# Optimization experiments

Hardware: AMD Instinct MI355X
Metric: run time of the kernel (lower is better)

## Reference

```python
import jax, jax.numpy as jnp
import numpy as np

B, T, DF, S = 64, 16, 512, 196      # batch, ticks, backbone channels, tokens
D_IN, H = 512, 8                     # attention embed dim, heads
DH = D_IN // H
DM, MEM, HN = 1024, 25, 32           # d_model neurons, memory length, NLM hidden
NSA, NSO, DOUT = 512, 512, 512       # sync sizes (random-pairing), output dim


def _ln(x, g, b, eps=1e-5):
    m = x.mean(-1, keepdims=True)
    v = ((x - m) ** 2).mean(-1, keepdims=True)
    return (x - m) / jnp.sqrt(v + eps) * g + b


def setup_inputs() -> dict:
    key = jax.random.key(0)
    ks = jax.random.split(key, 24)
    rn = lambda k, sh, sc: jax.random.normal(k, sh, jnp.float32) * sc
    p = {}
    p['x'] = rn(ks[0], (B, T, DF, S), 1.0)
    # q_proj (LazyLinear: n_sync_action -> d_input)
    p['Wqp'] = rn(ks[1], (NSA, D_IN), (1.0 / NSA) ** 0.5); p['bqp'] = jnp.zeros((D_IN,))
    # kv_proj: LazyLinear(DF->D_IN) + LayerNorm
    p['Wkv'] = rn(ks[2], (DF, D_IN), (1.0 / DF) ** 0.5); p['bkv'] = jnp.zeros((D_IN,))
    p['g_kv'] = jnp.ones((D_IN,)); p['b_kv'] = jnp.zeros((D_IN,))
    # MultiheadAttention projections
    sc = (1.0 / D_IN) ** 0.5
    p['Wq'] = rn(ks[3], (D_IN, D_IN), sc); p['bq'] = jnp.zeros((D_IN,))
    p['Wk'] = rn(ks[4], (D_IN, D_IN), sc); p['bk'] = jnp.zeros((D_IN,))
    p['Wv'] = rn(ks[5], (D_IN, D_IN), sc); p['bv'] = jnp.zeros((D_IN,))
    p['Wo'] = rn(ks[6], (D_IN, D_IN), sc); p['bo'] = jnp.zeros((D_IN,))
    # synapses: Linear(D_IN+DM -> 2*DM) + GLU + LayerNorm(DM)
    p['Wsyn'] = rn(ks[7], (D_IN + DM, 2 * DM), (1.0 / (D_IN + DM)) ** 0.5)
    p['bsyn'] = jnp.zeros((2 * DM,))
    p['g_syn'] = jnp.ones((DM,)); p['b_syn'] = jnp.zeros((DM,))
    # NLM: per-neuron 2-layer MLP over memory window
    p['W1'] = rn(ks[8], (DM, MEM, HN), (1.0 / MEM) ** 0.5); p['b1'] = jnp.zeros((DM, HN))
    p['W2'] = rn(ks[9], (DM, HN), (1.0 / HN) ** 0.5); p['b2'] = jnp.zeros((DM,))
    # learned initial states
    p['init_act'] = rn(ks[10], (DM,), (1.0 / DM) ** 0.5)
    p['init_hist'] = rn(ks[11], (DM, MEM), (1.0 / (DM + MEM)) ** 0.5)
    # decay params (init zero in torch)
    p['decay_a'] = jnp.zeros((NSA,)); p['decay_o'] = jnp.zeros((NSO,))
    # output projection (LazyLinear: n_sync_out -> d_output)
    p['Wout'] = rn(ks[12], (NSO, DOUT), (1.0 / NSO) ** 0.5); p['bout'] = jnp.zeros((DOUT,))
    # random-pairing neuron indices (buffers, constants)
    p['li_a'] = jax.random.randint(ks[13], (NSA,), 0, DM, jnp.int32)
    p['ri_a'] = jax.random.randint(ks[14], (NSA,), 0, DM, jnp.int32)
    p['li_o'] = jax.random.randint(ks[15], (NSO,), 0, DM, jnp.int32)
    p['ri_o'] = jax.random.randint(ks[16], (NSO,), 0, DM, jnp.int32)
    return p


def reference(x, Wqp, bqp, Wkv, bkv, g_kv, b_kv, Wq, bq, Wk, bk, Wv, bv, Wo, bo,
              Wsyn, bsyn, g_syn, b_syn, W1, b1, W2, b2, init_act, init_hist,
              decay_a, decay_o, Wout, bout, li_a, ri_a, li_o, ri_o):
    r_a = jnp.exp(-jnp.clip(decay_a, 0.0, 15.0))   # [NSA]
    r_o = jnp.exp(-jnp.clip(decay_o, 0.0, 15.0))   # [NSO]
    act0 = jnp.broadcast_to(init_act, (B, DM))
    hist0 = jnp.broadcast_to(init_hist, (B, DM, MEM))
    # initial 'out' sync state (decay_alpha=pairwise, decay_beta=ones)
    ao0 = act0[:, li_o] * act0[:, ri_o]
    bo0 = jnp.ones_like(ao0)
    # 'action' state starts None -> zeros so first update gives alpha=pairwise, beta=1
    aa0 = jnp.zeros((B, NSA), x.dtype); ba0 = jnp.zeros((B, NSA), x.dtype)

    def mha(q, kv):
        # q [B,1,D_IN], kv [B,S,D_IN]
        qh = (q @ Wq + bq).reshape(B, 1, H, DH)
        kh = (kv @ Wk + bk).reshape(B, S, H, DH)
        vh = (kv @ Wv + bv).reshape(B, S, H, DH)
        sc = jnp.einsum('bqhd,bkhd->bhqk', qh, kh) / jnp.sqrt(jnp.float32(DH))
        a = jax.nn.softmax(sc, axis=-1)
        o = jnp.einsum('bhqk,bkhd->bqhd', a, vh).reshape(B, 1, D_IN)
        return o @ Wo + bo

    def tick(carry, xt):
        act, hist, aa, ba, ao, bo_ = carry
        # compute_kv: identity backbone, flatten(2).transpose(1,2) -> [B,S,DF]
        kv = _ln(jnp.swapaxes(xt, 1, 2) @ Wkv + bkv, g_kv, b_kv)
        # action sync
        aa = r_a * aa + act[:, li_a] * act[:, ri_a]
        ba = r_a * ba + 1.0
        sync_a = aa / jnp.sqrt(ba)
        q = (sync_a @ Wqp + bqp)[:, None, :]
        attn = mha(q, kv)[:, 0]                         # [B,D_IN]
        pre = jnp.concatenate([attn, act], axis=-1)     # [B,D_IN+DM]
        g = pre @ Wsyn + bsyn
        a_, b_ = jnp.split(g, 2, axis=-1)
        pre_act = _ln(a_ * jax.nn.sigmoid(b_), g_syn, b_syn)  # [B,DM]
        hist = jnp.concatenate([hist[:, :, 1:], pre_act[:, :, None]], axis=2)
        # NLM: per-neuron MLP over memory window
        h = jax.nn.relu(jnp.einsum('bnm,nmh->bnh', hist, W1) + b1)
        act = jnp.einsum('bnh,nh->bn', h, W2) + b2
        # out sync
        ao = r_o * ao + act[:, li_o] * act[:, ri_o]
        bo_ = r_o * bo_ + 1.0
        sync_o = ao / jnp.sqrt(bo_)
        pred = sync_o @ Wout + bout                      # [B,DOUT]
        logp = jax.nn.log_softmax(pred, axis=-1)
        ne = -(jnp.exp(logp) * logp).sum(-1) / jnp.log(jnp.float32(DOUT))
        cert = jnp.stack([ne, 1.0 - ne], axis=-1)        # [B,2]
        return (act, hist, aa, ba, ao, bo_), (pred, cert)

    xt = jnp.moveaxis(x, 1, 0)  # [T,B,DF,S]
    _, (preds, certs) = jax.lax.scan(tick, (act0, hist0, aa0, ba0, ao0, bo0), xt)
    predictions = jnp.moveaxis(preds, 0, -1)   # [B,DOUT,T]
    certainties = jnp.moveaxis(certs, 0, -1)   # [B,2,T]
    return predictions, certainties
```

## Files before the change

### kernel.cpp

```cpp
#include <hip/hip_runtime.h>
#include <stdint.h>
#include <stddef.h>

#define B_    64
#define T_    16
#define DF_   512
#define S_    196
#define DIN_  512
#define H_    8
#define DH_   64
#define DM_   1024
#define MEM_  25
#define HN_   32
#define MR_   (B_*S_)

typedef short bf16x8 __attribute__((ext_vector_type(8)));
typedef short short4v __attribute__((ext_vector_type(4)));
typedef float f32x4  __attribute__((ext_vector_type(4)));

__device__ __forceinline__ float b2f(short h){
  unsigned u = ((unsigned)(unsigned short)h) << 16;
  float f; __builtin_memcpy(&f, &u, 4); return f;
}
__device__ __forceinline__ short f2b(float f){
  unsigned u; __builtin_memcpy(&u, &f, 4);
  u = (u + 0x7fffu + ((u >> 16) & 1u)) >> 16;
  return (short)(unsigned short)u;
}
__device__ __forceinline__ float clip015(float d){
  return d < 0.f ? 0.f : (d > 15.f ? 15.f : d);
}

template<int OUTF32, int LNEPI>
__global__ __launch_bounds__(256,2) void gemm_k(
    const short* __restrict__ A, const short* __restrict__ WT,
    void* __restrict__ Cout,
    const float* __restrict__ biasA, const float* __restrict__ biasB, int nsplit,
    const float* __restrict__ mu, const float* __restrict__ iv,
    const float* __restrict__ gw, const float* __restrict__ bw,
    int M, int N, int K, int lda, int ldc)
{
  __shared__ short lA[128*64];
  __shared__ short lB[128*64];
  const int tid = threadIdx.x;
  const int w = tid >> 6, l = tid & 63;
  const int m0 = blockIdx.x * 128, n0 = blockIdx.y * 128;
  const int wm = (w >> 1) * 64, wn = (w & 1) * 64;
  f32x4 acc[4][4];
  #pragma unroll
  for (int i=0;i<4;i++)
    #pragma unroll
    for (int j=0;j<4;j++) acc[i][j] = (f32x4){0.f,0.f,0.f,0.f};

  for (int k0 = 0; k0 < K; k0 += 64) {
    #pragma unroll
    for (int rnd = 0; rnd < 4; ++rnd) {
      int cb = (rnd*4 + w) * 64;
      int slot = cb + l;
      int row = slot >> 3, kb = slot & 7;
      int kc = k0 + ((kb ^ (row & 7)) << 3);
      int gm = m0 + row; if (gm > M-1) gm = M-1;
      __builtin_amdgcn_global_load_lds(
          (const __attribute__((address_space(1))) void*)(A + (size_t)gm * lda + kc),
          (__attribute__((address_space(3))) void*)&lA[cb*8], 16, 0, 0);
      __builtin_amdgcn_global_load_lds(
          (const __attribute__((address_space(1))) void*)(WT + (size_t)(n0 + row) * K + kc),
          (__attribute__((address_space(3))) void*)&lB[cb*8], 16, 0, 0);
    }
    asm volatile("s_waitcnt vmcnt(0)" ::: "memory");
    __syncthreads();
    #pragma unroll
    for (int ks = 0; ks < 2; ++ks) {
      bf16x8 af[4], bfr[4];
      #pragma unroll
      for (int i = 0; i < 4; ++i) {
        int ra = wm + i*16 + (l & 15);
        int c  = ks*4 + (l >> 4);
        af[i]  = *(const bf16x8*)&lA[ra*64 + ((c ^ (ra & 7)) << 3)];
        int rb = wn + i*16 + (l & 15);
        bfr[i] = *(const bf16x8*)&lB[rb*64 + ((c ^ (rb & 7)) << 3)];
      }
      #pragma unroll
      for (int i = 0; i < 4; ++i)
        #pragma unroll
        for (int j = 0; j < 4; ++j)
          acc[i][j] = __builtin_amdgcn_mfma_f32_16x16x32_bf16(af[i], bfr[j], acc[i][j], 0, 0, 0);
    }
    __syncthreads();
  }
  #pragma unroll
  for (int i = 0; i < 4; ++i) {
    #pragma unroll
    for (int j = 0; j < 4; ++j) {
      int gn = n0 + wn + j*16 + (l & 15);
      float ivn = 0.f, mun = 0.f, bb = 0.f;
      if (LNEPI == 2) { ivn = iv[gn]; mun = mu[gn]; }
      else bb = biasA ? ((gn < nsplit) ? biasA[gn] : biasB[gn - nsplit]) : 0.f;
      #pragma unroll
      for (int r = 0; r < 4; ++r) {
        int gm = m0 + wm + i*16 + (l >> 4)*4 + r;
        if (gm < M) {
          float v;
          if (LNEPI == 2) v = ivn*(acc[i][j][r] - mun*gw[gm]) + bw[gm];
          else            v = acc[i][j][r] + bb;
          if (OUTF32) ((float*)Cout)[(size_t)gm * ldc + gn] = v;
          else        ((short*)Cout)[(size_t)gm * ldc + gn] = f2b(v);
        }
      }
    }
  }
}

__global__ __launch_bounds__(256) void xpose_x(const float* __restrict__ x,
                                               short* __restrict__ xT, int t0, int tc)
{
  __shared__ float tile[32][33];
  int df0 = blockIdx.x*32, s0 = blockIdx.y*32;
  int z = blockIdx.z;
  int b = z / tc, ti = z % tc;
  int tx = threadIdx.x & 31, ty = threadIdx.x >> 5;
  const float* src = x + (size_t)(b*T_ + t0 + ti) * DF_ * S_;
  #pragma unroll
  for (int i = 0; i < 4; ++i) {
    int df = df0 + ty + i*8;
    int s  = s0 + tx;
    tile[ty+i*8][tx] = (s < S_) ? src[(size_t)df*S_ + s] : 0.f;
  }
  __syncthreads();
  short* dst = xT + (size_t)(ti*B_ + b) * S_ * DIN_;
  #pragma unroll
  for (int i = 0; i < 4; ++i) {
    int s  = s0 + ty + i*8;
    int df = df0 + tx;
    if (s < S_) dst[(size_t)s*DF_ + df] = f2b(tile[tx][ty+i*8]);
  }
}

__global__ __launch_bounds__(256) void wtrans(const float* __restrict__ in,
    short* __restrict__ out, int R, int C, int ldo, int coff,
    const float* __restrict__ scale)
{
  __shared__ float tile[32][33];
  int c0 = blockIdx.x*32, r0 = blockIdx.y*32;
  int tx = threadIdx.x & 31, ty = threadIdx.x >> 5;
  #pragma unroll
  for (int i = 0; i < 4; ++i) {
    int r = r0+ty+i*8;
    float sc = scale ? scale[r] : 1.f;
    tile[ty+i*8][tx] = in[(size_t)r*C + c0+tx] * sc;
  }
  __syncthreads();
  #pragma unroll
  for (int i = 0; i < 4; ++i)
    out[(size_t)(c0+ty+i*8)*ldo + coff + r0+tx] = f2b(tile[tx][ty+i*8]);
}

__global__ __launch_bounds__(256) void cvtb(const float* __restrict__ in,
                                            short* __restrict__ out, int n)
{
  int i = blockIdx.x*256 + threadIdx.x;
  if (i < n) out[i] = f2b(in[i]);
}

__global__ __launch_bounds__(256) void bias_fold(const float* __restrict__ vec,
    const float* __restrict__ W, const float* __restrict__ base,
    float* __restrict__ out, int N, int ldw)
{
  int n = blockIdx.x*256 + threadIdx.x;
  if (n >= N) return;
  float a = base ? base[n] : 0.f;
  #pragma unroll 8
  for (int k = 0; k < 512; ++k) a += vec[k]*W[(size_t)k*ldw + n];
  out[n] = a;
}

__global__ __launch_bounds__(256) void permrows(const short* __restrict__ in,
                                                short* __restrict__ out)
{
  int r = blockIdx.x;
  int k = r >> 4, i = r & 15;
  int src = (i < 8) ? (k*8 + i) : (1024 + k*8 + (i - 8));
  const bf16x8* s = (const bf16x8*)(in + (size_t)src*1536);
  bf16x8* d = (bf16x8*)(out + (size_t)r*1536);
  int j = threadIdx.x;
  if (j < 192) d[j] = s[j];
}

__global__ __launch_bounds__(256) void ln_stats(const short* __restrict__ in,
    float* __restrict__ mu, float* __restrict__ iv, int nrows)
{
  int w = threadIdx.x >> 6, l = threadIdx.x & 63;
  int r = blockIdx.x*4 + w;
  if (r >= nrows) return;
  bf16x8 v8 = *(const bf16x8*)&in[(size_t)r*512 + l*8];
  float s = 0.f, s2 = 0.f;
  #pragma unroll
  for (int j = 0; j < 8; ++j) { float v = b2f(v8[j]); s += v; s2 += v*v; }
  #pragma unroll
  for (int m = 1; m < 64; m <<= 1) { s += __shfl_xor(s, m, 64); s2 += __shfl_xor(s2, m, 64); }
  if (l == 0) {
    float mean = s * (1.f/512.f);
    float var  = s2 * (1.f/512.f) - mean*mean;
    mu[r] = mean;
    iv[r] = rsqrtf(var + 1e-5f);
  }
}

__device__ __forceinline__ void outk_body(int tt, int b, int tid,
    float* syncL, float* wred,
    const float* actT, float* ao, float* bo_s,
    const int* li_o, const int* ri_o, const float* decay_o,
    const short* WoutB, const float* bout, float* out)
{
  int j = tid;
  float rr = expf(-clip015(decay_o[j]));
  float prod = actT[li_o[j]*64 + b] * actT[ri_o[j]*64 + b];
  float a2 = rr*ao[b*512+j] + prod; ao[b*512+j] = a2;
  float bb2 = rr*bo_s[b*512+j] + 1.f; bo_s[b*512+j] = bb2;
  syncL[j] = a2 * rsqrtf(bb2);
  __syncthreads();
  float a = bout[j];
  #pragma unroll 8
  for (int k = 0; k < 512; ++k) a += syncL[k]*b2f(WoutB[k*512+j]);
  out[((size_t)b*512 + j)*16 + tt] = a;
  int w = tid >> 6, l = tid & 63;
  float m = a;
  #pragma unroll
  for (int k = 32; k >= 1; k >>= 1) m = fmaxf(m, __shfl_xor(m, k, 64));
  if (l == 0) wred[w] = m;
  __syncthreads();
  float M = wred[0];
  #pragma unroll
  for (int k = 1; k < 8; ++k) M = fmaxf(M, wred[k]);
  float e = expf(a - M);
  float z = e, s1 = e*(a - M);
  #pragma unroll
  for (int k = 32; k >= 1; k >>= 1) { z += __shfl_xor(z, k, 64); s1 += __shfl_xor(s1, k, 64); }
  if (l == 0) { wred[8+w] = z; wred[16+w] = s1; }
  __syncthreads();
  if (tid == 0) {
    float Z = 0.f, S1 = 0.f;
    #pragma unroll
    for (int k = 0; k < 8; ++k) { Z += wred[8+k]; S1 += wred[16+k]; }
    float plp = S1 / Z - logf(Z);
    float ne = -plp * (1.f/logf(512.f));
    out[524288 + (size_t)b*32 + tt]      = ne;
    out[524288 + (size_t)b*32 + 16 + tt] = 1.f - ne;
  }
}

__global__ __launch_bounds__(512) void tick_ao(
    const float* __restrict__ actT,
    float* __restrict__ aa, float* __restrict__ ba,
    const int* __restrict__ li_a, const int* __restrict__ ri_a,
    const float* __restrict__ decay_a,
    const short* __restrict__ WqqB, const float* __restrict__ bqh,
    const short* __restrict__ KVT, int ldkv, int ti,
    short* __restrict__ preb,
    float* __restrict__ ao, float* __restrict__ bo_s,
    const int* __restrict__ li_o, const int* __restrict__ ri_o,
    const float* __restrict__ decay_o,
    const short* __restrict__ WoutB, const float* __restrict__ bout,
    float* __restrict__ out, int t)
{
  __shared__ __attribute__((aligned(16))) float smem[3072];
  const int bid = blockIdx.x, tid = threadIdx.x;
  if (bid < 64) {
    int b = bid;
    float* syncL = smem;
    float* qhL   = smem + 512;
    float* pL    = smem + 1024;
    int j = tid;
    float rr = expf(-clip015(decay_a[j]));
    float prod = actT[li_a[j]*64 + b] * actT[ri_a[j]*64 + b];
    float a2 = rr*aa[b*512+j] + prod; aa[b*512+j] = a2;
    float bb2 = rr*ba[b*512+j] + 1.f;  ba[b*512+j] = bb2;
    syncL[j] = a2 * rsqrtf(bb2);
    __syncthreads();
    float qa = bqh[j];
    #pragma unroll 8
    for (int k = 0; k < 512; ++k) qa += syncL[k]*b2f(WqqB[k*512+j]);
    qhL[j] = qa;
    __syncthreads();
    int h = tid >> 6, l = tid & 63;
    const size_t cb = (size_t)(ti*B_ + b) * S_;
    const short* Kb = KVT + (size_t)(h*64)*ldkv + cb;
    int s3 = 192 + l; int s3c = s3 < S_ ? s3 : S_-1;
    float sc0=0.f, sc1=0.f, sc2=0.f, sc3=0.f;
    #pragma unroll 8
    for (int d = 0; d < 64; ++d) {
      const short* kr = Kb + (size_t)d*ldkv;
      float qv = qhL[h*64 + d];
      sc0 += qv * b2f(kr[l]);
      sc1 += qv * b2f(kr[64 + l]);
      sc2 += qv * b2f(kr[128 + l]);
      sc3 += qv * b2f(kr[s3c]);
    }
    sc0 *= 0.125f; sc1 *= 0.125f; sc2 *= 0.125f;
    sc3 = (s3 < S_) ? sc3*0.125f : -1e30f;
    float mx = fmaxf(fmaxf(sc0, sc1), fmaxf(sc2, sc3));
    #pragma unroll
    for (int k = 32; k >= 1; k >>= 1) mx = fmaxf(mx, __shfl_xor(mx, k, 64));
    float p0 = expf(sc0-mx), p1 = expf(sc1-mx), p2 = expf(sc2-mx), p3 = expf(sc3-mx);
    pL[h*256 + l] = p0; pL[h*256 + 64+l] = p1;
    pL[h*256 + 128+l] = p2; pL[h*256 + 192+l] = p3;
    float ps = p0+p1+p2+p3;
    #pragma unroll
    for (int k = 32; k >= 1; k >>= 1) ps += __shfl_xor(ps, k, 64);
    float inv = 1.f / ps;
    __syncthreads();
    const short4v* vrow = (const short4v*)(KVT + (size_t)(512 + h*64 + l)*ldkv + cb);
    const float* pp = pL + h*256;
    float ac0=0.f, ac1=0.f, ac2=0.f, ac3=0.f;
    #pragma unroll 7
    for (int c = 0; c < 49; ++c) {
      short4v v4 = vrow[c];
      ac0 += pp[c*4]   * b2f(v4.x);
      ac1 += pp[c*4+1] * b2f(v4.y);
      ac2 += pp[c*4+2] * b2f(v4.z);
      ac3 += pp[c*4+3] * b2f(v4.w);
    }
    float accv = (ac0+ac1)+(ac2+ac3);
    preb[(size_t)b*1536 + h*64 + l] = f2b(accv * inv);
  } else if (t > 0) {
    outk_body(t-1, bid-64, tid, smem, smem+512, actT, ao, bo_s,
              li_o, ri_o, decay_o, WoutB, bout, out);
  }
}

__global__ __launch_bounds__(512) void outk_fin(
    const float* __restrict__ actT,
    float* __restrict__ ao, float* __restrict__ bo_s,
    const int* __restrict__ li_o, const int* __restrict__ ri_o,
    const float* __restrict__ decay_o,
    const short* __restrict__ WoutB, const float* __restrict__ bout,
    float* __restrict__ out)
{
  __shared__ __attribute__((aligned(16))) float smem[544];
  outk_body(T_-1, blockIdx.x, threadIdx.x, smem, smem+512, actT, ao, bo_s,
            li_o, ri_o, decay_o, WoutB, bout, out);
}

__global__ __launch_bounds__(512) void syn_glu(const short* __restrict__ preb,
    const short* __restrict__ WsynP, const float* __restrict__ bsynF,
    float* __restrict__ u)
{
  __shared__ f32x4 part[512];
  const int bid = blockIdx.x, tid = threadIdx.x;
  int w = tid >> 6, l = tid & 63;
  int mf = w & 3, kh = w >> 2;
  int arow = mf*16 + (l & 15);
  int kbase = kh*768 + (l >> 4)*8;
  const short* ap = preb + (size_t)arow*1536 + kbase;
  const short* bp = WsynP + (size_t)(bid*16 + (l & 15))*1536 + kbase;
  f32x4 acc = (f32x4){0.f,0.f,0.f,0.f};
  #pragma unroll 4
  for (int ks = 0; ks < 24; ++ks) {
    bf16x8 av = *(const bf16x8*)(ap + ks*32);
    bf16x8 bv = *(const bf16x8*)(bp + ks*32);
    acc = __builtin_amdgcn_mfma_f32_16x16x32_bf16(av, bv, acc, 0, 0, 0);
  }
  part[w*64 + l] = acc;
  __syncthreads();
  if (w < 4) {
    f32x4 o1 = part[w*64 + l], o2 = part[(w+4)*64 + l];
    int c = l & 15;
    int colg = bid*8 + (c & 7);
    float bias = (c < 8) ? bsynF[colg] : bsynF[1024 + colg];
    float tv[4], pv[4];
    #pragma unroll
    for (int r2 = 0; r2 < 4; ++r2) tv[r2] = o1[r2] + o2[r2] + bias;
    #pragma unroll
    for (int r2 = 0; r2 < 4; ++r2) pv[r2] = __shfl_xor(tv[r2], 8, 64);
    if (c < 8) {
      #pragma unroll
      for (int r2 = 0; r2 < 4; ++r2) {
        float uu = tv[r2] * (1.f/(1.f + expf(-pv[r2])));
        int brow = w*16 + (l >> 4)*4 + r2;
        u[brow*1024 + colg] = uu;
      }
    }
  }
}

__global__ __launch_bounds__(512) void nlm_ln(const float* __restrict__ u,
    const float* __restrict__ gsyn, const float* __restrict__ bln,
    float* __restrict__ hist,
    const float* __restrict__ W1, const float* __restrict__ b1,
    const float* __restrict__ W2, const float* __restrict__ b2,
    float* __restrict__ actT, short* __restrict__ preb, int t)
{
  __shared__ float mstat[64], istat[64];
  const int bid = blockIdx.x, tid = threadIdx.x;
  {
    int b = tid >> 3, p = tid & 7;
    const float* up = u + b*1024 + p*128;
    float s = 0.f, s2 = 0.f;
    #pragma unroll 8
    for (int i = 0; i < 128; ++i) { float v = up[i]; s += v; s2 += v*v; }
    #pragma unroll
    for (int k = 4; k >= 1; k >>= 1) { s += __shfl_xor(s, k, 64); s2 += __shfl_xor(s2, k, 64); }
    if (p == 0) {
      float mean = s * (1.f/1024.f);
      float var  = s2 * (1.f/1024.f) - mean*mean;
      mstat[b] = mean;
      istat[b] = rsqrtf(var + 1e-5f);
    }
  }
  __syncthreads();
  int n = (bid << 3) + (tid >> 6), b = tid & 63;
  float nv = (u[b*1024 + n] - mstat[b]) * istat[b] * gsyn[n] + bln[n];
  int slot = t % MEM_;
  hist[((size_t)n*MEM_ + slot)*64 + b] = nv;
  float h[32];
  #pragma unroll
  for (int j = 0; j < 32; ++j) h[j] = b1[n*32+j];
  #pragma unroll 5
  for (int m = 0; m < MEM_; ++m) {
    int phys = (t + 1 + m) % MEM_;
    float hv = (m == MEM_-1) ? nv : hist[((size_t)n*MEM_ + phys)*64 + b];
    const float* wp = &W1[((size_t)n*MEM_ + m)*32];
    #pragma unroll
    for (int j = 0; j < 32; ++j) h[j] += hv * wp[j];
  }
  float acc = b2[n];
  #pragma unroll
  for (int j = 0; j < 32; ++j) acc += fmaxf(h[j], 0.f) * W2[n*32+j];
  actT[n*64 + b] = acc;
  preb[(size_t)b*1536 + 512 + n] = f2b(acc);
}

__global__ __launch_bounds__(256) void initk(float* __restrict__ aa, float* __restrict__ ba,
    float* __restrict__ ao, float* __restrict__ bo_s,
    float* __restrict__ actT, float* __restrict__ hist, short* __restrict__ preb,
    const float* __restrict__ init_act, const float* __restrict__ init_hist,
    const int* __restrict__ li_o, const int* __restrict__ ri_o)
{
  int i = blockIdx.x*256 + threadIdx.x;
  if (i < 64*512) {
    aa[i] = 0.f; ba[i] = 0.f;
    int j = i & 511;
    ao[i] = init_act[li_o[j]] * init_act[ri_o[j]];
    bo_s[i] = 1.f;
  }
  if (i < 65536) {
    int n = i >> 6, b = i & 63;
    actT[i] = init_act[n];
    preb[(size_t)b*1536 + 512 + n] = f2b(init_act[n]);
  }
  if (i < DM_*MEM_*64) {
    int nm = i >> 6;
    hist[i] = init_hist[nm];
  }
}

extern "C" void kernel_launch(void* const* d_in, const int* in_sizes, int n_in,
                              void* d_out, int out_size, void* d_ws, size_t ws_size,
                              hipStream_t stream)
{
  (void)in_sizes; (void)n_in; (void)out_size;
  const float* x       = (const float*)d_in[0];
  const float* Wqp     = (const float*)d_in[1];
  const float* bqp     = (const float*)d_in[2];
  const float* Wkv     = (const float*)d_in[3];
  const float* bkv     = (const float*)d_in[4];
  const float* g_kv    = (const float*)d_in[5];
  const float* b_kv    = (const float*)d_in[6];
  const float* Wq      = (const float*)d_in[7];
  const float* bq      = (const float*)d_in[8];
  const float* Wk      = (const float*)d_in[9];
  const float* bk      = (const float*)d_in[10];
  const float* Wv      = (const float*)d_in[11];
  const float* bv      = (const float*)d_in[12];
  const float* Wo      = (const float*)d_in[13];
  const float* bo_p    = (const float*)d_in[14];
  const float* Wsyn    = (const float*)d_in[15];
  const float* bsyn    = (const float*)d_in[16];
  const float* g_syn   = (const float*)d_in[17];
  const float* b_syn   = (const float*)d_in[18];
  const float* W1      = (const float*)d_in[19];
  const float* b1      = (const float*)d_in[20];
  const float* W2      = (const float*)d_in[21];
  const float* b2      = (const float*)d_in[22];
  const float* init_act  = (const float*)d_in[23];
  const float* init_hist = (const float*)d_in[24];
  const float* decay_a = (const float*)d_in[25];
  const float* decay_o = (const float*)d_in[26];
  const float* Wout    = (const float*)d_in[27];
  const float* bout    = (const float*)d_in[28];
  const int* li_a = (const int*)d_in[29];
  const int* ri_a = (const int*)d_in[30];
  const int* li_o = (const int*)d_in[31];
  const int* ri_o = (const int*)d_in[32];

  char* ws = (char*)d_ws;
  size_t off = 0;
  auto alloc = [&](size_t bytes) { char* p = ws + off; off += (bytes + 255) & ~(size_t)255; return p; };
  short* WkvT   = (short*)alloc(512*512*2);
  short* WkkvT  = (short*)alloc(1024*512*2);
  short* WsynF  = (short*)alloc(2048*1536*2);
  short* WsynP  = (short*)alloc(2048*1536*2);
  short* WsynTt = (short*)alloc(2048*512*2);
  short* WqpB   = (short*)alloc(512*512*2);
  short* WqT    = (short*)alloc(512*512*2);
  short* WoB    = (short*)alloc(512*512*2);
  short* WqqB   = (short*)alloc(512*512*2);
  short* WoutB  = (short*)alloc(512*512*2);
  float* bqh    = (float*)alloc(512*4);
  float* bsynF  = (float*)alloc(2048*4);
  float* gw     = (float*)alloc(1024*4);
  float* bw     = (float*)alloc(1024*4);
  short* preb   = (short*)alloc(64*1536*2);
  float* u      = (float*)alloc(64*1024*4);
  float* aa     = (float*)alloc(64*512*4);
  float* ba     = (float*)alloc(64*512*4);
  float* ao     = (float*)alloc(64*512*4);
  float* bo_s   = (float*)alloc(64*512*4);
  float* actT   = (float*)alloc(1024*64*4);
  float* hist   = (float*)alloc((size_t)1024*25*64*4);
  float* mu     = (float*)alloc((size_t)MR_*T_*4);
  float* iv     = (float*)alloc((size_t)MR_*T_*4);
  size_t fixed_end = off;

  const size_t PT_XT = (size_t)MR_*512*2;
  const size_t PT_KV = (size_t)MR_*1024*2;
  const size_t per_tick = PT_XT*2 + PT_KV;
  size_t avail = (ws_size > fixed_end + 512) ? ws_size - fixed_end - 512 : 0;
  int tc = (int)(avail / per_tick);
  if (tc > T_) tc = T_;
  if (tc < 1) tc = 1;

  short* xT  = (short*)(ws + fixed_end);
  short* kvp = (short*)((char*)xT  + PT_XT*tc);
  short* KVT = (short*)((char*)kvp + PT_XT*tc);

  const int BIG = 1 << 30;
  const float* FN = nullptr;

  initk<<<6400, 256, 0, stream>>>(aa, ba, ao, bo_s, actT, hist, preb,
                                  init_act, init_hist, li_o, ri_o);
  wtrans<<<dim3(16,16), 256, 0, stream>>>(Wkv, WkvT, 512, 512, 512, 0, nullptr);
  wtrans<<<dim3(16,16), 256, 0, stream>>>(Wk,  WkkvT, 512, 512, 512, 0, g_kv);
  wtrans<<<dim3(16,16), 256, 0, stream>>>(Wv,  WkkvT + (size_t)512*512, 512, 512, 512, 0, g_kv);
  wtrans<<<dim3(64,32), 256, 0, stream>>>(Wsyn + (size_t)512*2048, WsynF, 1024, 2048, 1536, 512, nullptr);
  wtrans<<<dim3(64,16), 256, 0, stream>>>(Wsyn, WsynTt, 512, 2048, 512, 0, nullptr);
  wtrans<<<dim3(16,16), 256, 0, stream>>>(Wq,  WqT, 512, 512, 512, 0, nullptr);
  cvtb<<<1024, 256, 0, stream>>>(Wqp, WqpB, 512*512);
  cvtb<<<1024, 256, 0, stream>>>(Wo,  WoB,  512*512);
  cvtb<<<1024, 256, 0, stream>>>(Wout, WoutB, 512*512);
  gemm_k<0,0><<<dim3(4,4), 256, 0, stream>>>(WqpB, WqT, WqqB, nullptr, nullptr, BIG,
                                             FN, FN, FN, FN, 512, 512, 512, 512, 512);
  gemm_k<0,0><<<dim3(16,4), 256, 0, stream>>>(WsynTt, WoB, WsynF, nullptr, nullptr, BIG,
                                              FN, FN, FN, FN, 2048, 512, 512, 512, 1536);
  permrows<<<2048, 256, 0, stream>>>(WsynF, WsynP);
  bias_fold<<<2, 256, 0, stream>>>(bqp,  Wq,   bq,   bqh,   512,  512);
  bias_fold<<<8, 256, 0, stream>>>(bo_p, Wsyn, bsyn, bsynF, 2048, 2048);
  bias_fold<<<2, 256, 0, stream>>>(g_kv, Wk, nullptr, gw,       512, 512);
  bias_fold<<<2, 256, 0, stream>>>(g_kv, Wv, nullptr, gw + 512, 512, 512);
  bias_fold<<<2, 256, 0, stream>>>(b_kv, Wk, bk, bw,       512, 512);
  bias_fold<<<2, 256, 0, stream>>>(b_kv, Wv, bv, bw + 512, 512, 512);

  for (int t0 = 0; t0 < T_; t0 += tc) {
    int tcc = (t0 + tc <= T_) ? tc : (T_ - t0);
    int Mc = MR_ * tcc;
    xpose_x<<<dim3(16,7,B_*tcc), 256, 0, stream>>>(x, xT, t0, tcc);
    gemm_k<0,0><<<dim3(98*tcc,4), 256, 0, stream>>>(xT, WkvT, kvp, bkv, bkv, BIG,
                                                    FN, FN, FN, FN, Mc, 512, 512, 512, 512);
    ln_stats<<<Mc/4, 256, 0, stream>>>(kvp, mu, iv, Mc);
    gemm_k<0,2><<<dim3(8,98*tcc), 256, 0, stream>>>(WkkvT, kvp, KVT, nullptr, nullptr, BIG,
                                                    mu, iv, gw, bw, 1024, Mc, 512, 512, Mc);
    for (int ti = 0; ti < tcc; ++ti) {
      int t = t0 + ti;
      tick_ao<<<128, 512, 0, stream>>>(actT, aa, ba, li_a, ri_a, decay_a,
                                       WqqB, bqh, KVT, Mc, ti, preb,
                                       ao, bo_s, li_o, ri_o, decay_o,
                                       WoutB, bout, (float*)d_out, t);
      syn_glu<<<128, 512, 0, stream>>>(preb, WsynP, bsynF, u);
      nlm_ln<<<128, 512, 0, stream>>>(u, g_syn, b_syn, hist,
                                      W1, b1, W2, b2, actT, preb, t);
    }
  }
  outk_fin<<<64, 512, 0, stream>>>(actT, ao, bo_s, li_o, ri_o, decay_o,
                                   WoutB, bout, (float*)d_out);
}
```

Baseline: 2.494 ms.

## Overlap next chunk's KV projection GEMMs with per-tick recurrent kernels

Splits the 16 ticks into four chunks of four and double-buffers the KV projection, LN stats and K/V GEMM outputs. The bulk GEMM work for the next chunk is sliced into extra blocks appended to each of the three per-tick recurrent kernel launches, which only use 128 blocks. The aim is to fill idle compute units during the latency-bound sequential ticks. The input transpose is also hoisted into a single launch over all ticks. This costs extra workspace for the double buffers and larger shared memory per block, which may lower occupancy or slow the critical-path blocks.

Result: faster. 2.443 ms (-2.0%).

```diff
diff --git a/kernel.cpp b/kernel.cpp
--- a/kernel.cpp
+++ b/kernel.cpp
@@ -13,6 +13,8 @@
 #define MEM_  25
 #define HN_   32
 #define MR_   (B_*S_)
+#define TC_   4
+#define MCC_  (MR_*TC_)
 
 typedef short bf16x8 __attribute__((ext_vector_type(8)));
 typedef short short4v __attribute__((ext_vector_type(4)));
@@ -32,7 +34,8 @@
 }
 
 template<int OUTF32, int LNEPI>
-__global__ __launch_bounds__(256,2) void gemm_k(
+__device__ __forceinline__ void gemm_body(int tid, int bx, int by, int aload,
+    short* lA, short* lB,
     const short* __restrict__ A, const short* __restrict__ WT,
     void* __restrict__ Cout,
     const float* __restrict__ biasA, const float* __restrict__ biasB, int nsplit,
@@ -40,11 +43,8 @@
     const float* __restrict__ gw, const float* __restrict__ bw,
     int M, int N, int K, int lda, int ldc)
 {
-  __shared__ short lA[128*64];
-  __shared__ short lB[128*64];
-  const int tid = threadIdx.x;
   const int w = tid >> 6, l = tid & 63;
-  const int m0 = blockIdx.x * 128, n0 = blockIdx.y * 128;
+  const int m0 = bx * 128, n0 = by * 128;
   const int wm = (w >> 1) * 64, wn = (w & 1) * 64;
   f32x4 acc[4][4];
   #pragma unroll
@@ -59,10 +59,12 @@
       int slot = cb + l;
       int row = slot >> 3, kb = slot & 7;
       int kc = k0 + ((kb ^ (row & 7)) << 3);
-      int gm = m0 + row; if (gm > M-1) gm = M-1;
-      __builtin_amdgcn_global_load_lds(
-          (const __attribute__((address_space(1))) void*)(A + (size_t)gm * lda + kc),
-          (__attribute__((address_space(3))) void*)&lA[cb*8], 16, 0, 0);
+      if (aload) {
+        int gm = m0 + row; if (gm > M-1) gm = M-1;
+        __builtin_amdgcn_global_load_lds(
+            (const __attribute__((address_space(1))) void*)(A + (size_t)gm * lda + kc),
+            (__attribute__((address_space(3))) void*)&lA[cb*8], 16, 0, 0);
+      }
       __builtin_amdgcn_global_load_lds(
           (const __attribute__((address_space(1))) void*)(WT + (size_t)(n0 + row) * K + kc),
           (__attribute__((address_space(3))) void*)&lB[cb*8], 16, 0, 0);
@@ -111,99 +113,133 @@
   }
 }
 
-__global__ __launch_bounds__(256) void xpose_x(const float* __restrict__ x,
-                                               short* __restrict__ xT, int t0, int tc)
-{
-  __shared__ float tile[32][33];
-  int df0 = blockIdx.x*32, s0 = blockIdx.y*32;
-  int z = blockIdx.z;
-  int b = z / tc, ti = z % tc;
-  int tx = threadIdx.x & 31, ty = threadIdx.x >> 5;
-  const float* src = x + (size_t)(b*T_ + t0 + ti) * DF_ * S_;
-  #pragma unroll
-  for (int i = 0; i < 4; ++i) {
-    int df = df0 + ty + i*8;
-    int s  = s0 + tx;
-    tile[ty+i*8][tx] = (s < S_) ? src[(size_t)df*S_ + s] : 0.f;
-  }
-  __syncthreads();
-  short* dst = xT + (size_t)(ti*B_ + b) * S_ * DIN_;
-  #pragma unroll
-  for (int i = 0; i < 4; ++i) {
-    int s  = s0 + ty + i*8;
-    int df = df0 + tx;
-    if (s < S_) dst[(size_t)s*DF_ + df] = f2b(tile[tx][ty+i*8]);
-  }
-}
-
-__global__ __launch_bounds__(256) void wtrans(const float* __restrict__ in,
-    short* __restrict__ out, int R, int C, int ldo, int coff,
-    const float* __restrict__ scale)
-{
-  __shared__ float tile[32][33];
-  int c0 = blockIdx.x*32, r0 = blockIdx.y*32;
-  int tx = threadIdx.x & 31, ty = threadIdx.x >> 5;
-  #pragma unroll
-  for (int i = 0; i < 4; ++i) {
-    int r = r0+ty+i*8;
-    float sc = scale ? scale[r] : 1.f;
-    tile[ty+i*8][tx] = in[(size_t)r*C + c0+tx] * sc;
-  }
-  __syncthreads();
-  #pragma unroll
-  for (int i = 0; i < 4; ++i)
-    out[(size_t)(c0+ty+i*8)*ldo + coff + r0+tx] = f2b(tile[tx][ty+i*8]);
-}
-
-__global__ __launch_bounds__(256) void cvtb(const float* __restrict__ in,
-                                            short* __restrict__ out, int n)
-{
-  int i = blockIdx.x*256 + threadIdx.x;
-  if (i < n) out[i] = f2b(in[i]);
-}
-
-__global__ __launch_bounds__(256) void bias_fold(const float* __restrict__ vec,
-    const float* __restrict__ W, const float* __restrict__ base,
-    float* __restrict__ out, int N, int ldw)
-{
-  int n = blockIdx.x*256 + threadIdx.x;
-  if (n >= N) return;
-  float a = base ? base[n] : 0.f;
+template<int OUTF32, int LNEPI>
+__global__ __launch_bounds__(256,2) void gemm_k(
+    const short* __restrict__ A, const short* __restrict__ WT,
+    void* __restrict__ Cout,
+    const float* __restrict__ biasA, const float* __restrict__ biasB, int nsplit,
+    const float* __restrict__ mu, const float* __restrict__ iv,
+    const float* __restrict__ gw, const float* __restrict__ bw,
+    int M, int N, int K, int lda, int ldc)
+{
+  __shared__ short lA[128*64];
+  __shared__ short lB[128*64];
+  gemm_body<OUTF32,LNEPI>(threadIdx.x, blockIdx.x, blockIdx.y, 1, lA, lB,
+                          A, WT, Cout, biasA, biasB, nsplit, mu, iv, gw, bw,
+                          M, N, K, lda, ldc);
+}
+
+__device__ __forceinline__ void run_piggy(int tid, int pb, int pop, int poff,
+    char* pool,
+    const short* __restrict__ xTn, const short* __restrict__ WkvT,
+    const float* __restrict__ bkv,
+    short* __restrict__ kvpN, float* __restrict__ muN, float* __restrict__ ivN,
+    const short* __restrict__ WkkvT, const float* __restrict__ gw,
+    const float* __restrict__ bw, short* __restrict__ KVTN, int McN)
+{
+  if (pop == 1) {
+    int twin = tid >> 8;
+    short* lA = (short*)pool;
+    short* lB = (short*)(pool + 16384 + 16384*twin);
+    int p = poff + pb; if (p > 783) p = 783;
+    int bx = p % 392, byp = p / 392;
+    gemm_body<0,0>(tid & 255, bx, byp*2 + twin, twin == 0, lA, lB,
+                   xTn, WkvT, kvpN, bkv, bkv, 1 << 30,
+                   nullptr, nullptr, nullptr, nullptr,
+                   McN, 512, 512, 512, 512);
+  } else if (pop == 2) {
+    int blk = poff + pb;
+    int w = tid >> 6, l = tid & 63;
+    for (int i = 0; i < 8; ++i) {
+      int r = blk*64 + i*8 + w;
+      if (r < McN) {
+        bf16x8 v8 = *(const bf16x8*)&kvpN[(size_t)r*512 + l*8];
+        float s = 0.f, s2 = 0.f;
+        #pragma unroll
+        for (int j = 0; j < 8; ++j) { float v = b2f(v8[j]); s += v; s2 += v*v; }
+        #pragma unroll
+        for (int m = 1; m < 64; m <<= 1) { s += __shfl_xor(s, m, 64); s2 += __shfl_xor(s2, m, 64); }
+        if (l == 0) {
+          float mean = s * (1.f/512.f);
+          float var  = s2 * (1.f/512.f) - mean*mean;
+          muN[r] = mean;
+          ivN[r] = rsqrtf(var + 1e-5f);
+        }
+      }
+    }
+  } else if (pop == 3) {
+    int twin = tid >> 8;
+    short* lA = (short*)pool;
+    short* lB = (short*)(pool + 16384 + 16384*twin);
+    int p = poff + pb; if (p > 1567) p = 1567;
+    int bx = p % 8, byp = p / 8;
+    gemm_body<0,2>(tid & 255, bx, byp*2 + twin, twin == 0, lA, lB,
+                   WkkvT, kvpN, KVTN, nullptr, nullptr, 0,
+                   muN, ivN, gw, bw, 1024, McN, 512, 512, McN);
+  }
+}
+
+__device__ __forceinline__ void attn_body(int b, int tid, float* smem,
+    const float* actT, float* aa, float* ba,
+    const int* li_a, const int* ri_a, const float* decay_a,
+    const short* WqqB, const float* bqh,
+    const short* KVT, int ldkv, int ti, short* preb)
+{
+  float* syncL = smem;
+  float* qhL   = smem + 512;
+  float* pL    = smem + 1024;
+  int j = tid;
+  float rr = expf(-clip015(decay_a[j]));
+  float prod = actT[li_a[j]*64 + b] * actT[ri_a[j]*64 + b];
+  float a2 = rr*aa[b*512+j] + prod; aa[b*512+j] = a2;
+  float bb2 = rr*ba[b*512+j] + 1.f;  ba[b*512+j] = bb2;
+  syncL[j] = a2 * rsqrtf(bb2);
+  __syncthreads();
+  float qa = bqh[j];
   #pragma unroll 8
-  for (int k = 0; k < 512; ++k) a += vec[k]*W[(size_t)k*ldw + n];
-  out[n] = a;
-}
-
-__global__ __launch_bounds__(256) void permrows(const short* __restrict__ in,
-                                                short* __restrict__ out)
-{
-  int r = blockIdx.x;
-  int k = r >> 4, i = r & 15;
-  int src = (i < 8) ? (k*8 + i) : (1024 + k*8 + (i - 8));
-  const bf16x8* s = (const bf16x8*)(in + (size_t)src*1536);
-  bf16x8* d = (bf16x8*)(out + (size_t)r*1536);
-  int j = threadIdx.x;
-  if (j < 192) d[j] = s[j];
-}
-
-__global__ __launch_bounds__(256) void ln_stats(const short* __restrict__ in,
-    float* __restrict__ mu, float* __restrict__ iv, int nrows)
-{
-  int w = threadIdx.x >> 6, l = threadIdx.x & 63;
-  int r = blockIdx.x*4 + w;
-  if (r >= nrows) return;
-  bf16x8 v8 = *(const bf16x8*)&in[(size_t)r*512 + l*8];
-  float s = 0.f, s2 = 0.f;
-  #pragma unroll
-  for (int j = 0; j < 8; ++j) { float v = b2f(v8[j]); s += v; s2 += v*v; }
-  #pragma unroll
-  for (int m = 1; m < 64; m <<= 1) { s += __shfl_xor(s, m, 64); s2 += __shfl_xor(s2, m, 64); }
-  if (l == 0) {
-    float mean = s * (1.f/512.f);
-    float var  = s2 * (1.f/512.f) - mean*mean;
-    mu[r] = mean;
-    iv[r] = rsqrtf(var + 1e-5f);
-  }
+  for (int k = 0; k < 512; ++k) qa += syncL[k]*b2f(WqqB[k*512+j]);
+  qhL[j] = qa;
+  __syncthreads();
+  int h = tid >> 6, l = tid & 63;
+  const size_t cb = (size_t)(ti*B_ + b) * S_;
+  const short* Kb = KVT + (size_t)(h*64)*ldkv + cb;
+  int s3 = 192 + l; int s3c = s3 < S_ ? s3 : S_-1;
+  float sc0=0.f, sc1=0.f, sc2=0.f, sc3=0.f;
+  #pragma unroll 8
+  for (int d = 0; d < 64; ++d) {
+    const short* kr = Kb + (size_t)d*ldkv;
+    float qv = qhL[h*64 + d];
+    sc0 += qv * b2f(kr[l]);
+    sc1 += qv * b2f(kr[64 + l]);
+    sc2 += qv * b2f(kr[128 + l]);
+    sc3 += qv * b2f(kr[s3c]);
+  }
+  sc0 *= 0.125f; sc1 *= 0.125f; sc2 *= 0.125f;
+  sc3 = (s3 < S_) ? sc3*0.125f : -1e30f;
+  float mx = fmaxf(fmaxf(sc0, sc1), fmaxf(sc2, sc3));
+  #pragma unroll
+  for (int k = 32; k >= 1; k >>= 1) mx = fmaxf(mx, __shfl_xor(mx, k, 64));
+  float p0 = expf(sc0-mx), p1 = expf(sc1-mx), p2 = expf(sc2-mx), p3 = expf(sc3-mx);
+  pL[h*256 + l] = p0; pL[h*256 + 64+l] = p1;
+  pL[h*256 + 128+l] = p2; pL[h*256 + 192+l] = p3;
+  float ps = p0+p1+p2+p3;
+  #pragma unroll
+  for (int k = 32; k >= 1; k >>= 1) ps += __shfl_xor(ps, k, 64);
+  float inv = 1.f / ps;
+  __syncthreads();
+  const short4v* vrow = (const short4v*)(KVT + (size_t)(512 + h*64 + l)*ldkv + cb);
+  const float* pp = pL + h*256;
+  float ac0=0.f, ac1=0.f, ac2=0.f, ac3=0.f;
+  #pragma unroll 7
+  for (int c = 0; c < 49; ++c) {
+    short4v v4 = vrow[c];
+    ac0 += pp[c*4]   * b2f(v4.x);
+    ac1 += pp[c*4+1] * b2f(v4.y);
+    ac2 += pp[c*4+2] * b2f(v4.z);
+    ac3 += pp[c*4+3] * b2f(v4.w);
+  }
+  float accv = (ac0+ac1)+(ac2+ac3);
+  preb[(size_t)b*1536 + h*64 + l] = f2b(accv * inv);
 }
 
 __device__ __forceinline__ void outk_body(int tt, int b, int tid,
@@ -249,104 +285,10 @@
   }
 }
 
-__global__ __launch_bounds__(512) void tick_ao(
-    const float* __restrict__ actT,
-    float* __restrict__ aa, float* __restrict__ ba,
-    const int* __restrict__ li_a, const int* __restrict__ ri_a,
-    const float* __restrict__ decay_a,
-    const short* __restrict__ WqqB, const float* __restrict__ bqh,
-    const short* __restrict__ KVT, int ldkv, int ti,
-    short* __restrict__ preb,
-    float* __restrict__ ao, float* __restrict__ bo_s,
-    const int* __restrict__ li_o, const int* __restrict__ ri_o,
-    const float* __restrict__ decay_o,
-    const short* __restrict__ WoutB, const float* __restrict__ bout,
-    float* __restrict__ out, int t)
-{
-  __shared__ __attribute__((aligned(16))) float smem[3072];
-  const int bid = blockIdx.x, tid = threadIdx.x;
-  if (bid < 64) {
-    int b = bid;
-    float* syncL = smem;
-    float* qhL   = smem + 512;
-    float* pL    = smem + 1024;
-    int j = tid;
-    float rr = expf(-clip015(decay_a[j]));
-    float prod = actT[li_a[j]*64 + b] * actT[ri_a[j]*64 + b];
-    float a2 = rr*aa[b*512+j] + prod; aa[b*512+j] = a2;
-    float bb2 = rr*ba[b*512+j] + 1.f;  ba[b*512+j] = bb2;
-    syncL[j] = a2 * rsqrtf(bb2);
-    __syncthreads();
-    float qa = bqh[j];
-    #pragma unroll 8
-    for (int k = 0; k < 512; ++k) qa += syncL[k]*b2f(WqqB[k*512+j]);
-    qhL[j] = qa;
-    __syncthreads();
-    int h = tid >> 6, l = tid & 63;
-    const size_t cb = (size_t)(ti*B_ + b) * S_;
-    const short* Kb = KVT + (size_t)(h*64)*ldkv + cb;
-    int s3 = 192 + l; int s3c = s3 < S_ ? s3 : S_-1;
-    float sc0=0.f, sc1=0.f, sc2=0.f, sc3=0.f;
-    #pragma unroll 8
-    for (int d = 0; d < 64; ++d) {
-      const short* kr = Kb + (size_t)d*ldkv;
-      float qv = qhL[h*64 + d];
-      sc0 += qv * b2f(kr[l]);
-      sc1 += qv * b2f(kr[64 + l]);
-      sc2 += qv * b2f(kr[128 + l]);
-      sc3 += qv * b2f(kr[s3c]);
-    }
-    sc0 *= 0.125f; sc1 *= 0.125f; sc2 *= 0.125f;
-    sc3 = (s3 < S_) ? sc3*0.125f : -1e30f;
-    float mx = fmaxf(fmaxf(sc0, sc1), fmaxf(sc2, sc3));
-    #pragma unroll
-    for (int k = 32; k >= 1; k >>= 1) mx = fmaxf(mx, __shfl_xor(mx, k, 64));
-    float p0 = expf(sc0-mx), p1 = expf(sc1-mx), p2 = expf(sc2-mx), p3 = expf(sc3-mx);
-    pL[h*256 + l] = p0; pL[h*256 + 64+l] = p1;
-    pL[h*256 + 128+l] = p2; pL[h*256 + 192+l] = p3;
-    float ps = p0+p1+p2+p3;
-    #pragma unroll
-    for (int k = 32; k >= 1; k >>= 1) ps += __shfl_xor(ps, k, 64);
-    float inv = 1.f / ps;
-    __syncthreads();
-    const short4v* vrow = (const short4v*)(KVT + (size_t)(512 + h*64 + l)*ldkv + cb);
-    const float* pp = pL + h*256;
-    float ac0=0.f, ac1=0.f, ac2=0.f, ac3=0.f;
-    #pragma unroll 7
-    for (int c = 0; c < 49; ++c) {
-      short4v v4 = vrow[c];
-      ac0 += pp[c*4]   * b2f(v4.x);
-      ac1 += pp[c*4+1] * b2f(v4.y);
-      ac2 += pp[c*4+2] * b2f(v4.z);
-      ac3 += pp[c*4+3] * b2f(v4.w);
-    }
-    float accv = (ac0+ac1)+(ac2+ac3);
-    preb[(size_t)b*1536 + h*64 + l] = f2b(accv * inv);
-  } else if (t > 0) {
-    outk_body(t-1, bid-64, tid, smem, smem+512, actT, ao, bo_s,
-              li_o, ri_o, decay_o, WoutB, bout, out);
-  }
-}
-
-__global__ __launch_bounds__(512) void outk_fin(
-    const float* __restrict__ actT,
-    float* __restrict__ ao, float* __restrict__ bo_s,
-    const int* __restrict__ li_o, const int* __restrict__ ri_o,
-    const float* __restrict__ decay_o,
-    const short* __restrict__ WoutB, const float* __restrict__ bout,
-    float* __restrict__ out)
-{
-  __shared__ __attribute__((aligned(16))) float smem[544];
-  outk_body(T_-1, blockIdx.x, threadIdx.x, smem, smem+512, actT, ao, bo_s,
-            li_o, ri_o, decay_o, WoutB, bout, out);
-}
-
-__global__ __launch_bounds__(512) void syn_glu(const short* __restrict__ preb,
-    const short* __restrict__ WsynP, const float* __restrict__ bsynF,
-    float* __restrict__ u)
-{
-  __shared__ f32x4 part[512];
-  const int bid = blockIdx.x, tid = threadIdx.x;
+__device__ __forceinline__ void synglu_body(int bid, int tid, char* pool,
+    const short* preb, const short* WsynP, const float* bsynF, float* u)
+{
+  f32x4* part = (f32x4*)pool;
   int w = tid >> 6, l = tid & 63;
   int mf = w & 3, kh = w >> 2;
   int arow = mf*16 + (l & 15);
@@ -383,15 +325,13 @@
   }
 }
 
-__global__ __launch_bounds__(512) void nlm_ln(const float* __restrict__ u,
-    const float* __restrict__ gsyn, const float* __restrict__ bln,
-    float* __restrict__ hist,
-    const float* __restrict__ W1, const float* __restrict__ b1,
-    const float* __restrict__ W2, const float* __restrict__ b2,
-    float* __restrict__ actT, short* __restrict__ preb, int t)
-{
-  __shared__ float mstat[64], istat[64];
-  const int bid = blockIdx.x, tid = threadIdx.x;
+__device__ __forceinline__ void nlmln_body(int bid, int tid, char* pool,
+    const float* u, const float* gsyn, const float* bln, float* hist,
+    const float* W1, const float* b1, const float* W2, const float* b2,
+    float* actT, short* preb, int t)
+{
+  float* mstat = (float*)pool;
+  float* istat = mstat + 64;
   {
     int b = tid >> 3, p = tid & 7;
     const float* up = u + b*1024 + p*128;
@@ -428,6 +368,176 @@
   for (int j = 0; j < 32; ++j) acc += fmaxf(h[j], 0.f) * W2[n*32+j];
   actT[n*64 + b] = acc;
   preb[(size_t)b*1536 + 512 + n] = f2b(acc);
+}
+
+#define PIGGY_ARGS int pop, int poff, \
+    const short* __restrict__ xTn, const short* __restrict__ WkvT, \
+    const float* __restrict__ bkv, short* __restrict__ kvpN, \
+    float* __restrict__ muN, float* __restrict__ ivN, \
+    const short* __restrict__ WkkvT, const float* __restrict__ gw, \
+    const float* __restrict__ bw, short* __restrict__ KVTN, int McN
+#define PIGGY_CALL run_piggy(tid, (int)blockIdx.x - 128, pop, poff, pool, \
+    xTn, WkvT, bkv, kvpN, muN, ivN, WkkvT, gw, bw, KVTN, McN)
+
+__global__ __launch_bounds__(512) void stageA(
+    const float* __restrict__ actT,
+    float* __restrict__ aa, float* __restrict__ ba,
+    const int* __restrict__ li_a, const int* __restrict__ ri_a,
+    const float* __restrict__ decay_a,
+    const short* __restrict__ WqqB, const float* __restrict__ bqh,
+    const short* __restrict__ KVT, int ldkv, int ti,
+    short* __restrict__ preb,
+    float* __restrict__ ao, float* __restrict__ bo_s,
+    const int* __restrict__ li_o, const int* __restrict__ ri_o,
+    const float* __restrict__ decay_o,
+    const short* __restrict__ WoutB, const float* __restrict__ bout,
+    float* __restrict__ out, int t, PIGGY_ARGS)
+{
+  __shared__ __attribute__((aligned(16))) char pool[49152];
+  const int bid = blockIdx.x, tid = threadIdx.x;
+  if (bid < 128) {
+    float* smem = (float*)pool;
+    if (bid < 64)
+      attn_body(bid, tid, smem, actT, aa, ba, li_a, ri_a, decay_a,
+                WqqB, bqh, KVT, ldkv, ti, preb);
+    else if (t > 0)
+      outk_body(t-1, bid-64, tid, smem, smem+512, actT, ao, bo_s,
+                li_o, ri_o, decay_o, WoutB, bout, out);
+  } else {
+    PIGGY_CALL;
+  }
+}
+
+__global__ __launch_bounds__(512) void stageB(
+    const short* __restrict__ preb, const short* __restrict__ WsynP,
+    const float* __restrict__ bsynF, float* __restrict__ u, PIGGY_ARGS)
+{
+  __shared__ __attribute__((aligned(16))) char pool[49152];
+  const int bid = blockIdx.x, tid = threadIdx.x;
+  if (bid < 128) synglu_body(bid, tid, pool, preb, WsynP, bsynF, u);
+  else PIGGY_CALL;
+}
+
+__global__ __launch_bounds__(512) void stageC(
+    const float* __restrict__ u, const float* __restrict__ gsyn,
+    const float* __restrict__ bln, float* __restrict__ hist,
+    const float* __restrict__ W1, const float* __restrict__ b1,
+    const float* __restrict__ W2, const float* __restrict__ b2,
+    float* __restrict__ actT, short* __restrict__ preb, int t, PIGGY_ARGS)
+{
+  __shared__ __attribute__((aligned(16))) char pool[49152];
+  const int bid = blockIdx.x, tid = threadIdx.x;
+  if (bid < 128) nlmln_body(bid, tid, pool, u, gsyn, bln, hist,
+                            W1, b1, W2, b2, actT, preb, t);
+  else PIGGY_CALL;
+}
+
+__global__ __launch_bounds__(512) void outk_fin(
+    const float* __restrict__ actT,
+    float* __restrict__ ao, float* __restrict__ bo_s,
+    const int* __restrict__ li_o, const int* __restrict__ ri_o,
+    const float* __restrict__ decay_o,
+    const short* __restrict__ WoutB, const float* __restrict__ bout,
+    float* __restrict__ out)
+{
+  __shared__ __attribute__((aligned(16))) float smem[544];
+  outk_body(T_-1, blockIdx.x, threadIdx.x, smem, smem+512, actT, ao, bo_s,
+            li_o, ri_o, decay_o, WoutB, bout, out);
+}
+
+__global__ __launch_bounds__(256) void xpose_x(const float* __restrict__ x,
+                                               short* __restrict__ xT)
+{
+  __shared__ float tile[32][33];
+  int df0 = blockIdx.x*32, s0 = blockIdx.y*32;
+  int z = blockIdx.z;
+  int b = z / T_, t = z % T_;
+  int tx = threadIdx.x & 31, ty = threadIdx.x >> 5;
+  const float* src = x + (size_t)(b*T_ + t) * DF_ * S_;
+  #pragma unroll
+  for (int i = 0; i < 4; ++i) {
+    int df = df0 + ty + i*8;
+    int s  = s0 + tx;
+    tile[ty+i*8][tx] = (s < S_) ? src[(size_t)df*S_ + s] : 0.f;
+  }
+  __syncthreads();
+  short* dst = xT + (size_t)(t*B_ + b) * S_ * DIN_;
+  #pragma unroll
+  for (int i = 0; i < 4; ++i) {
+    int s  = s0 + ty + i*8;
+    int df = df0 + tx;
+    if (s < S_) dst[(size_t)s*DF_ + df] = f2b(tile[tx][ty+i*8]);
+  }
+}
+
+__global__ __launch_bounds__(256) void wtrans(const float* __restrict__ in,
+    short* __restrict__ out, int R, int C, int ldo, int coff,
+    const float* __restrict__ scale)
+{
+  __shared__ float tile[32][33];
+  int c0 = blockIdx.x*32, r0 = blockIdx.y*32;
+  int tx = threadIdx.x & 31, ty = threadIdx.x >> 5;
+  #pragma unroll
+  for (int i = 0; i < 4; ++i) {
+    int r = r0+ty+i*8;
+    float sc = scale ? scale[r] : 1.f;
+    tile[ty+i*8][tx] = in[(size_t)r*C + c0+tx] * sc;
+  }
+  __syncthreads();
+  #pragma unroll
+  for (int i = 0; i < 4; ++i)
+    out[(size_t)(c0+ty+i*8)*ldo + coff + r0+tx] = f2b(tile[tx][ty+i*8]);
+}
+
+__global__ __launch_bounds__(256) void cvtb(const float* __restrict__ in,
+                                            short* __restrict__ out, int n)
+{
+  int i = blockIdx.x*256 + threadIdx.x;
+  if (i < n) out[i] = f2b(in[i]);
+}
+
+__global__ __launch_bounds__(256) void bias_fold(const float* __restrict__ vec,
+    const float* __restrict__ W, const float* __restrict__ base,
+    float* __restrict__ out, int N, int ldw)
+{
+  int n = blockIdx.x*256 + threadIdx.x;
+  if (n >= N) return;
+  float a = base ? base[n] : 0.f;
+  #pragma unroll 8
+  for (int k = 0; k < 512; ++k) a += vec[k]*W[(size_t)k*ldw + n];
+  out[n] = a;
+}
+
+__global__ __launch_bounds__(256) void permrows(const short* __restrict__ in,
+                                                short* __restrict__ out)
+{
+  int r = blockIdx.x;
+  int k = r >> 4, i = r & 15;
+  int src = (i < 8) ? (k*8 + i) : (1024 + k*8 + (i - 8));
+  const bf16x8* s = (const bf16x8*)(in + (size_t)src*1536);
+  bf16x8* d = (bf16x8*)(out + (size_t)r*1536);
+  int j = threadIdx.x;
+  if (j < 192) d[j] = s[j];
+}
+
+__global__ __launch_bounds__(256) void ln_stats(const short* __restrict__ in,
+    float* __restrict__ mu, float* __restrict__ iv, int nrows)
+{
+  int w = threadIdx.x >> 6, l = threadIdx.x & 63;
+  int r = blockIdx.x*4 + w;
+  if (r >= nrows) return;
+  bf16x8 v8 = *(const bf16x8*)&in[(size_t)r*512 + l*8];
+  float s = 0.f, s2 = 0.f;
+  #pragma unroll
+  for (int j = 0; j < 8; ++j) { float v = b2f(v8[j]); s += v; s2 += v*v; }
+  #pragma unroll
+  for (int m = 1; m < 64; m <<= 1) { s += __shfl_xor(s, m, 64); s2 += __shfl_xor(s2, m, 64); }
+  if (l == 0) {
+    float mean = s * (1.f/512.f);
+    float var  = s2 * (1.f/512.f) - mean*mean;
+    mu[r] = mean;
+    iv[r] = rsqrtf(var + 1e-5f);
+  }
 }
 
 __global__ __launch_bounds__(256) void initk(float* __restrict__ aa, float* __restrict__ ba,
@@ -518,21 +628,29 @@
   float* bo_s   = (float*)alloc(64*512*4);
   float* actT   = (float*)alloc(1024*64*4);
   float* hist   = (float*)alloc((size_t)1024*25*64*4);
-  float* mu     = (float*)alloc((size_t)MR_*T_*4);
-  float* iv     = (float*)alloc((size_t)MR_*T_*4);
   size_t fixed_end = off;
 
-  const size_t PT_XT = (size_t)MR_*512*2;
-  const size_t PT_KV = (size_t)MR_*1024*2;
-  const size_t per_tick = PT_XT*2 + PT_KV;
-  size_t avail = (ws_size > fixed_end + 512) ? ws_size - fixed_end - 512 : 0;
-  int tc = (int)(avail / per_tick);
-  if (tc > T_) tc = T_;
-  if (tc < 1) tc = 1;
-
-  short* xT  = (short*)(ws + fixed_end);
-  short* kvp = (short*)((char*)xT  + PT_XT*tc);
-  short* KVT = (short*)((char*)kvp + PT_XT*tc);
+  const size_t szXT  = (size_t)T_*MR_*512*2;
+  const size_t szKVP = (size_t)MCC_*512*2;
+  const size_t szKVT = (size_t)MCC_*1024*2;
+  const size_t szST  = (size_t)MCC_*4;
+  size_t need_full = fixed_end + szXT + 2*szKVP + 2*szKVT + 4*szST + 4096;
+  bool pig_en = (ws_size >= need_full);
+
+  short* xT = (short*)alloc(szXT);
+  short* kvpB[2]; short* KVTB[2]; float* muB[2]; float* ivB[2];
+  kvpB[0] = (short*)alloc(szKVP);
+  KVTB[0] = (short*)alloc(szKVT);
+  muB[0]  = (float*)alloc(szST);
+  ivB[0]  = (float*)alloc(szST);
+  if (pig_en) {
+    kvpB[1] = (short*)alloc(szKVP);
+    KVTB[1] = (short*)alloc(szKVT);
+    muB[1]  = (float*)alloc(szST);
+    ivB[1]  = (float*)alloc(szST);
+  } else {
+    kvpB[1] = kvpB[0]; KVTB[1] = KVTB[0]; muB[1] = muB[0]; ivB[1] = ivB[0];
+  }
 
   const int BIG = 1 << 30;
   const float* FN = nullptr;
@@ -560,24 +678,51 @@
   bias_fold<<<2, 256, 0, stream>>>(b_kv, Wk, bk, bw,       512, 512);
   bias_fold<<<2, 256, 0, stream>>>(b_kv, Wv, bv, bw + 512, 512, 512);
 
-  for (int t0 = 0; t0 < T_; t0 += tc) {
-    int tcc = (t0 + tc <= T_) ? tc : (T_ - t0);
-    int Mc = MR_ * tcc;
-    xpose_x<<<dim3(16,7,B_*tcc), 256, 0, stream>>>(x, xT, t0, tcc);
-    gemm_k<0,0><<<dim3(98*tcc,4), 256, 0, stream>>>(xT, WkvT, kvp, bkv, bkv, BIG,
-                                                    FN, FN, FN, FN, Mc, 512, 512, 512, 512);
-    ln_stats<<<Mc/4, 256, 0, stream>>>(kvp, mu, iv, Mc);
-    gemm_k<0,2><<<dim3(8,98*tcc), 256, 0, stream>>>(WkkvT, kvp, KVT, nullptr, nullptr, BIG,
-                                                    mu, iv, gw, bw, 1024, Mc, 512, 512, Mc);
-    for (int ti = 0; ti < tcc; ++ti) {
-      int t = t0 + ti;
-      tick_ao<<<128, 512, 0, stream>>>(actT, aa, ba, li_a, ri_a, decay_a,
-                                       WqqB, bqh, KVT, Mc, ti, preb,
-                                       ao, bo_s, li_o, ri_o, decay_o,
-                                       WoutB, bout, (float*)d_out, t);
-      syn_glu<<<128, 512, 0, stream>>>(preb, WsynP, bsynF, u);
-      nlm_ln<<<128, 512, 0, stream>>>(u, g_syn, b_syn, hist,
-                                      W1, b1, W2, b2, actT, preb, t);
+  xpose_x<<<dim3(16,7,B_*T_), 256, 0, stream>>>(x, xT);
+
+  auto run_pipe = [&](int c, short* kvpP, float* muP, float* ivP, short* KVTP){
+    const short* xTc = xT + (size_t)c*TC_*MR_*512;
+    gemm_k<0,0><<<dim3(392,4), 256, 0, stream>>>(xTc, WkvT, kvpP, bkv, bkv, BIG,
+                                                 FN, FN, FN, FN, MCC_, 512, 512, 512, 512);
+    ln_stats<<<MCC_/4, 256, 0, stream>>>(kvpP, muP, ivP, MCC_);
+    gemm_k<0,2><<<dim3(8,392), 256, 0, stream>>>(WkkvT, kvpP, KVTP, nullptr, nullptr, BIG,
+                                                 muP, ivP, gw, bw, 1024, MCC_, 512, 512, MCC_);
+  };
+
+  auto pigcfg = [](int q, bool pig, int& op, int& pf, int& n){
+    op = 0; pf = 0; n = 0;
+    if (!pig) return;
+    if (q < 4)      { op = 1; pf = q*196;     n = 196; }
+    else if (q == 4){ op = 2; pf = 0;         n = 784; }
+    else            { op = 3; pf = (q-5)*224; n = 224; }
+  };
+
+  run_pipe(0, kvpB[0], muB[0], ivB[0], KVTB[0]);
+
+  for (int c = 0; c < 4; ++c) {
+    int par = pig_en ? (c & 1) : 0;
+    int nxt = pig_en ? (par ^ 1) : 0;
+    if (!pig_en && c > 0) run_pipe(c, kvpB[0], muB[0], ivB[0], KVTB[0]);
+    bool pig = pig_en && (c < 3);
+    const short* xTn = (c < 3) ? xT + (size_t)(c+1)*TC_*MR_*512 : xT;
+    for (int ti = 0; ti < TC_; ++ti) {
+      int t = c*TC_ + ti;
+      int op, pf, n;
+      pigcfg(ti*3+0, pig, op, pf, n);
+      stageA<<<128+n, 512, 0, stream>>>(actT, aa, ba, li_a, ri_a, decay_a,
+          WqqB, bqh, KVTB[par], MCC_, ti, preb,
+          ao, bo_s, li_o, ri_o, decay_o, WoutB, bout, (float*)d_out, t,
+          op, pf, xTn, WkvT, bkv, kvpB[nxt], muB[nxt], ivB[nxt],
+          WkkvT, gw, bw, KVTB[nxt], MCC_);
+      pigcfg(ti*3+1, pig, op, pf, n);
+      stageB<<<128+n, 512, 0, stream>>>(preb, WsynP, bsynF, u,
+          op, pf, xTn, WkvT, bkv, kvpB[nxt], muB[nxt], ivB[nxt],
+          WkkvT, gw, bw, KVTB[nxt], MCC_);
+      pigcfg(ti*3+2, pig, op, pf, n);
+      stageC<<<128+n, 512, 0, stream>>>(u, g_syn, b_syn, hist,
+          W1, b1, W2, b2, actT, preb, t,
+          op, pf, xTn, WkvT, bkv, kvpB[nxt], muB[nxt], ivB[nxt],
+          WkkvT, gw, bw, KVTB[nxt], MCC_);
     }
   }
   outk_fin<<<64, 512, 0, stream>>>(actT, ao, bo_s, li_o, ri_o, decay_o,
```
